# Performance work log

Measured on AMD Instinct MI355X. Metric: run time of the kernel, lower is better.

Reference implementation:

```python
import jax, jax.numpy as jnp
import numpy as np

D_MODEL = 1024
D_HEAD = 64


def setup_inputs() -> dict:
    key = jax.random.key(0)
    k_x, k_q, k_k, k_v, k_o = jax.random.split(key, 5)
    scale = 1.0 / np.sqrt(D_MODEL)
    residual_stream = jax.random.normal(k_x, (4, 2048, D_MODEL), dtype=jnp.float32)
    Q = scale * jax.random.normal(k_q, (D_MODEL, D_HEAD), dtype=jnp.float32)
    K = scale * jax.random.normal(k_k, (D_MODEL, D_HEAD), dtype=jnp.float32)
    V = scale * jax.random.normal(k_v, (D_MODEL, D_HEAD), dtype=jnp.float32)
    O = scale * jax.random.normal(k_o, (D_MODEL, D_HEAD), dtype=jnp.float32)
    return {"residual_stream": residual_stream, "Q": Q, "K": K, "V": V, "O": O}


def reference(residual_stream, Q, K, V, O) -> jnp.ndarray:
    # queries/keys: [B, S, d_head]
    queries = jnp.einsum('bsd,dh->bsh', residual_stream, Q)
    keys = jnp.einsum('bsd,dh->bsh', residual_stream, K)
    # NOTE: original module applies NO 1/sqrt(d_head) scaling.
    pre_attention = jnp.einsum('bqh,bkh->bqk', queries, keys)  # [B, S, S]
    S = pre_attention.shape[-1]
    causal = jnp.tril(jnp.ones((S, S), dtype=bool))
    pre_attention = jnp.where(causal[None], pre_attention, -jnp.inf)
    attention = jax.nn.softmax(pre_attention, axis=-1)
    # x = residual @ V @ O^T : [B, S, d_model]
    x = jnp.einsum('bsd,dh,eh->bse', residual_stream, V, O)
    return jnp.einsum('bqk,bke->bqe', attention, x)
```

## Files before the change

kernel.cpp:

```cpp
#include <hip/hip_runtime.h>
#include <hip/hip_bf16.h>
#include <math.h>

#define BATCH 4
#define SEQ   2048
#define DM    1024
#define DH    64
#define NROWS (BATCH*SEQ)
#define PVSPLIT 8

typedef __hip_bfloat16 bf16;
typedef __attribute__((ext_vector_type(8))) short short8;
typedef __attribute__((ext_vector_type(8))) unsigned short ushortx8;
typedef __attribute__((ext_vector_type(4))) float floatx4;

__device__ __forceinline__ ushort f2bf(float f) {
    union { bf16 h; ushort u; } cv;
    cv.h = __float2bfloat16(f);
    return cv.u;
}
__device__ __forceinline__ float bf2f(ushort u) {
    union { unsigned int i; float f; } v; v.i = ((unsigned int)u) << 16; return v.f;
}

__device__ __forceinline__ void load_lds16(const ushort* g, ushort* l) {
    __builtin_amdgcn_global_load_lds(
        (const __attribute__((address_space(1))) unsigned int*)g,
        (__attribute__((address_space(3))) unsigned int*)l, 16, 0, 0);
}

__global__ __launch_bounds__(256) void wprep_kernel(
    const float* __restrict__ Q, const float* __restrict__ K,
    const float* __restrict__ V, const float* __restrict__ O,
    ushort* __restrict__ WhT, ushort* __restrict__ WlT,
    ushort* __restrict__ Oh, ushort* __restrict__ Ol)
{
    int n = blockIdx.x;
    if (n < 192) {
        const float* W = (n < 64) ? Q : (n < 128) ? K : V;
        int c = n & 63;
        for (int k = threadIdx.x; k < DM; k += 256) {
            float w = W[k * DH + c];
            ushort hi = f2bf(w);
            WhT[n * DM + k] = hi;
            WlT[n * DM + k] = f2bf(w - bf2f(hi));
        }
    } else {
        int e0 = (n - 192) << 4;
        for (int idx = threadIdx.x; idx < 16 * DH; idx += 256) {
            int off = (e0 << 6) + idx;
            float w = O[off];
            ushort hi = f2bf(w);
            Oh[off] = hi;
            Ol[off] = f2bf(w - bf2f(hi));
        }
    }
}

__global__ __launch_bounds__(256) void qkv_part_kernel(
    const float* __restrict__ x, const ushort* __restrict__ WhT,
    const ushort* __restrict__ WlT, float* __restrict__ Cpart)
{
    __shared__ __align__(16) ushort Xs[2][32][34];
    __shared__ __align__(16) ushort Ws[2][192][34];
    int s0 = blockIdx.x * 32;
    int kb = blockIdx.y * 256;
    int t = threadIdx.x;
    int wave = t >> 6, lane = t & 63, m_ = lane & 15, qd = lane >> 4;
    const floatx4 z4 = {0.f, 0.f, 0.f, 0.f};
    floatx4 accq[2] = {z4, z4}, acck[2] = {z4, z4}, accv[2] = {z4, z4};
    int xr = t >> 3, xc = (t & 7) * 4;
    for (int k0 = 0; k0 < 256; k0 += 32) {
        float4 v = *(const float4*)&x[(size_t)(s0 + xr) * DM + kb + k0 + xc];
        ushort h0 = f2bf(v.x), h1 = f2bf(v.y), h2 = f2bf(v.z), h3 = f2bf(v.w);
        *(ushort4*)&Xs[0][xr][xc] = make_ushort4(h0, h1, h2, h3);
        *(ushort4*)&Xs[1][xr][xc] = make_ushort4(
            f2bf(v.x - bf2f(h0)), f2bf(v.y - bf2f(h1)),
            f2bf(v.z - bf2f(h2)), f2bf(v.w - bf2f(h3)));
        #pragma unroll
        for (int j = 0; j < 3; ++j) {
            int idx = t + j * 256, n = idx >> 2, kc = (idx & 3) * 8;
            *(uint4*)&Ws[0][n][kc] = *(const uint4*)&WhT[n * DM + kb + k0 + kc];
            *(uint4*)&Ws[1][n][kc] = *(const uint4*)&WlT[n * DM + kb + k0 + kc];
        }
        __syncthreads();
        short8 ah[2], al[2];
        #pragma unroll
        for (int mi = 0; mi < 2; ++mi) {
            ah[mi] = *(const short8*)&Xs[0][mi * 16 + m_][qd * 8];
            al[mi] = *(const short8*)&Xs[1][mi * 16 + m_][qd * 8];
        }
        int nq = wave * 16 + m_, nk = 64 + wave * 16 + m_, nv = 128 + wave * 16 + m_;
        short8 bqh = *(const short8*)&Ws[0][nq][qd * 8];
        short8 bql = *(const short8*)&Ws[1][nq][qd * 8];
        short8 bkh = *(const short8*)&Ws[0][nk][qd * 8];
        short8 bkl = *(const short8*)&Ws[1][nk][qd * 8];
        short8 bvh = *(const short8*)&Ws[0][nv][qd * 8];
        #pragma unroll
        for (int mi = 0; mi < 2; ++mi) {
            accq[mi] = __builtin_amdgcn_mfma_f32_16x16x32_bf16(ah[mi], bqh, accq[mi], 0, 0, 0);
            accq[mi] = __builtin_amdgcn_mfma_f32_16x16x32_bf16(al[mi], bqh, accq[mi], 0, 0, 0);
            accq[mi] = __builtin_amdgcn_mfma_f32_16x16x32_bf16(ah[mi], bql, accq[mi], 0, 0, 0);
            acck[mi] = __builtin_amdgcn_mfma_f32_16x16x32_bf16(ah[mi], bkh, acck[mi], 0, 0, 0);
            acck[mi] = __builtin_amdgcn_mfma_f32_16x16x32_bf16(al[mi], bkh, acck[mi], 0, 0, 0);
            acck[mi] = __builtin_amdgcn_mfma_f32_16x16x32_bf16(ah[mi], bkl, acck[mi], 0, 0, 0);
            accv[mi] = __builtin_amdgcn_mfma_f32_16x16x32_bf16(ah[mi], bvh, accv[mi], 0, 0, 0);
        }
        __syncthreads();
    }
    float* Cp = Cpart + (size_t)blockIdx.y * (NROWS * 192);
    #pragma unroll
    for (int mi = 0; mi < 2; ++mi) {
        #pragma unroll
        for (int r = 0; r < 4; ++r) {
            int row = s0 + mi * 16 + qd * 4 + r;
            float* base = Cp + (size_t)row * 192;
            base[wave * 16 + m_]       = accq[mi][r];
            base[64 + wave * 16 + m_]  = acck[mi][r];
            base[128 + wave * 16 + m_] = accv[mi][r];
        }
    }
}

__global__ __launch_bounds__(256) void qkv_reduce_kernel(
    const float* __restrict__ Cpart,
    ushort* __restrict__ qh, ushort* __restrict__ ql,
    ushort* __restrict__ kh, ushort* __restrict__ kl, ushort* __restrict__ xvP)
{
    __shared__ ushort xvs[32][72];
    const size_t SL = (size_t)NROWS * 192;
    int row0 = blockIdx.x * 32;
    int t = threadIdx.x;
    #pragma unroll
    for (int i = 0; i < 24; ++i) {
        int e = i * 256 + t;
        int r = e / 192, c = e - r * 192;
        size_t row = row0 + r;
        size_t off = row * 192 + c;
        float s = Cpart[off] + Cpart[SL + off] + Cpart[2 * SL + off] + Cpart[3 * SL + off];
        ushort hi = f2bf(s);
        if (c < 64) {
            qh[row * 64 + c] = hi; ql[row * 64 + c] = f2bf(s - bf2f(hi));
        } else if (c < 128) {
            kh[row * 64 + c - 64] = hi; kl[row * 64 + c - 64] = f2bf(s - bf2f(hi));
        } else {
            xvs[r][c - 128] = hi;
        }
    }
    __syncthreads();
    int h = t & 63, qd = t >> 6;
    ushortx8 v;
    #pragma unroll
    for (int j = 0; j < 8; ++j)
        v[j] = xvs[4 * qd + (j & 3) + ((j >> 2) << 4)][h];
    int b = row0 >> 11, c32 = (row0 & 2047) >> 5;
    *(ushortx8*)&xvP[((((size_t)b << 6) + c32) * 4 + qd) * 512 + h * 8] = v;
}

__global__ __launch_bounds__(512) void attn_part_kernel(
    const ushort* __restrict__ qh, const ushort* __restrict__ ql,
    const ushort* __restrict__ kh, const ushort* __restrict__ kl,
    const ushort* __restrict__ xvP,
    float* __restrict__ Opart, float* __restrict__ lpart)
{
    __shared__ __align__(16) ushort Kbuf[2][8192];
    __shared__ __align__(16) ushort xvbuf[2][4096];
    __shared__ float lred[2][2][16];
    int bid = blockIdx.x;
    int pp = bid & 63, b = (bid >> 6) & 3, s = bid >> 8;
    int srowA = pp << 4, srowB = (127 - pp) << 4;
    int t = threadIdx.x, wave = t >> 6, lane = t & 63, m_ = lane & 15, qd = lane >> 4;
    int nA = (pp >> 2) + 1, nB = ((127 - pp) >> 2) + 1;
    int tile = wave >> 2, h2 = (wave >> 1) & 1, nh = wave & 1;
    int srow = tile ? srowB : srowA;
    int nT = tile ? nB : nA;
    int jB = (nB - s + 3) >> 2;
    const ushort* khb = kh + (((size_t)b << 11)) * 64;
    const ushort* klb = kl + (((size_t)b << 11)) * 64;
    const ushort* xvPb = xvP + ((size_t)b << 17);
    short8 bq[2][2];
    {
        size_t qr = (size_t)((b << 11) + srow + m_) * 64 + qd * 8;
        bq[0][0] = *(const short8*)&qh[qr];
        bq[0][1] = *(const short8*)&qh[qr + 32];
        bq[1][0] = *(const short8*)&ql[qr];
        bq[1][1] = *(const short8*)&ql[qr + 32];
    }
    int drow = lane >> 3;
    int dlc = ((lane & 7) ^ drow) * 8;
    #define AT_STAGE(cc, buf)                                                   \
        { int k0r_ = (cc) << 6;                                                 \
          _Pragma("unroll")                                                     \
          for (int i_ = 0; i_ < 3; ++i_) {                                      \
              int c_ = wave * 3 + i_;                                           \
              if (c_ < 8)                                                       \
                  load_lds16(khb + (size_t)(k0r_ + c_ * 8 + drow) * 64 + dlc,   \
                             &Kbuf[buf][c_ * 512]);                             \
              else if (c_ < 16)                                                 \
                  load_lds16(klb + (size_t)(k0r_ + (c_ - 8) * 8 + drow) * 64 + dlc, \
                             &Kbuf[buf][4096 + (c_ - 8) * 512]);                \
              else                                                              \
                  load_lds16(xvPb + (size_t)(cc) * 4096 + (c_ - 16) * 512 + lane * 8, \
                             &xvbuf[buf][(c_ - 16) * 512]);                     \
          } }
    const floatx4 z4 = {0.f, 0.f, 0.f, 0.f};
    floatx4 accO[2] = {z4, z4};
    float ll = 0.f;
    int qrow = srow + m_;
    AT_STAGE(s, 0)
    for (int j = 0; j < jB; ++j) {
        int c = s + 4 * j;
        __syncthreads();
        if (j + 1 < jB) AT_STAGE(s + 4 * (j + 1), (j + 1) & 1)
        if (c < nT) {
            int bufi = j & 1;
            floatx4 accS[2] = {z4, z4};
            #pragma unroll
            for (int kk = 0; kk < 2; ++kk) {
                #pragma unroll
                for (int tt = 0; tt < 2; ++tt) {
                    int row = (2 * h2 + tt) * 16 + m_;
                    int chunk = ((kk << 2) + qd) ^ (m_ & 7);
                    const ushort* ph = &Kbuf[bufi][row * 64 + chunk * 8];
                    short8 akh = *(const short8*)ph;
                    short8 akl = *(const short8*)(ph + 4096);
                    accS[tt] = __builtin_amdgcn_mfma_f32_16x16x32_bf16(akh, bq[0][kk], accS[tt], 0, 0, 0);
                    accS[tt] = __builtin_amdgcn_mfma_f32_16x16x32_bf16(akl, bq[0][kk], accS[tt], 0, 0, 0);
                    accS[tt] = __builtin_amdgcn_mfma_f32_16x16x32_bf16(akh, bq[1][kk], accS[tt], 0, 0, 0);
                }
            }
            float lsum = 0.f;
            short8 pa;
            #pragma unroll
            for (int tt = 0; tt < 2; ++tt) {
                #pragma unroll
                for (int r = 0; r < 4; ++r) {
                    int kc = c * 64 + (2 * h2 + tt) * 16 + qd * 4 + r;
                    float p = (kc <= qrow) ? __expf(accS[tt][r]) : 0.f;
                    lsum += p;
                    pa[tt * 4 + r] = (short)f2bf(p);
                }
            }
            if (nh == 0) ll += lsum;
            const ushort* Xb = &xvbuf[bufi][(h2 * 4 + qd) * 512];
            #pragma unroll
            for (int i = 0; i < 2; ++i) {
                int h = (nh * 2 + i) * 16 + m_;
                short8 xv = *(const short8*)&Xb[h * 8];
                accO[i] = __builtin_amdgcn_mfma_f32_16x16x32_bf16(pa, xv, accO[i], 0, 0, 0);
            }
        }
    }
    ll += __shfl_xor(ll, 16); ll += __shfl_xor(ll, 32);
    if (qd == 0 && nh == 0) lred[tile][h2][m_] = ll;
    __syncthreads();
    if (t < 32) {
        int tl = t >> 4, q = t & 15;
        int row = (b << 11) + (tl ? srowB : srowA) + q;
        lpart[(size_t)s * NROWS + row] = lred[tl][0][q] + lred[tl][1][q];
    }
    float* OP = Opart + ((size_t)(s * 2 + h2) * NROWS + (b << 11) + srow) * 64;
    #pragma unroll
    for (int i = 0; i < 2; ++i)
        #pragma unroll
        for (int r = 0; r < 4; ++r)
            OP[(qd * 4 + r) * 64 + (nh * 2 + i) * 16 + m_] = accO[i][r];
    #undef AT_STAGE
}

__global__ __launch_bounds__(256) void axv_reduce_kernel(
    const float* __restrict__ AxvPart, const float* __restrict__ lpart,
    ushort* __restrict__ Axvh, ushort* __restrict__ Axvl)
{
    const size_t PSL = (size_t)NROWS * DH;
    int idx = blockIdx.x * 256 + threadIdx.x;
    size_t e = (size_t)idx * 4;
    int r = (int)(e >> 6);
    float4 a = *(const float4*)&AxvPart[e];
    #pragma unroll
    for (int sp = 1; sp < PVSPLIT; ++sp) {
        float4 v = *(const float4*)&AxvPart[sp * PSL + e];
        a.x += v.x; a.y += v.y; a.z += v.z; a.w += v.w;
    }
    float sc = 1.f / (lpart[r] + lpart[NROWS + r]
                    + lpart[2 * NROWS + r] + lpart[3 * NROWS + r]);
    a.x *= sc; a.y *= sc; a.z *= sc; a.w *= sc;
    ushort h0 = f2bf(a.x), h1 = f2bf(a.y), h2 = f2bf(a.z), h3 = f2bf(a.w);
    *(ushort4*)&Axvh[e] = make_ushort4(h0, h1, h2, h3);
    *(ushort4*)&Axvl[e] = make_ushort4(
        f2bf(a.x - bf2f(h0)), f2bf(a.y - bf2f(h1)),
        f2bf(a.z - bf2f(h2)), f2bf(a.w - bf2f(h3)));
}

__global__ __launch_bounds__(256) void out_kernel(
    const ushort* __restrict__ Axvh, const ushort* __restrict__ Axvl,
    const ushort* __restrict__ Oh, const ushort* __restrict__ Ol,
    float* __restrict__ out)
{
    __shared__ __align__(16) ushort As[2][64][72];
    __shared__ __align__(16) ushort Bsh[2][128][72];
    int bid = blockIdx.x;
    int r0 = (bid >> 3) << 6;
    int e0 = (bid & 7) << 7;
    int t = threadIdx.x;
    {
        int tr = t >> 2, tc = (t & 3) << 4;
        const ushort* ah = Axvh + (size_t)(r0 + tr) * DH + tc;
        const ushort* al = Axvl + (size_t)(r0 + tr) * DH + tc;
        *(uint4*)&As[0][tr][tc]     = *(const uint4*)ah;
        *(uint4*)&As[0][tr][tc + 8] = *(const uint4*)(ah + 8);
        *(uint4*)&As[1][tr][tc]     = *(const uint4*)al;
        *(uint4*)&As[1][tr][tc + 8] = *(const uint4*)(al + 8);
    }
    {
        int tr = t >> 1, tc = (t & 1) << 5;
        const ushort* bh = Oh + (size_t)(e0 + tr) * DH + tc;
        const ushort* bl = Ol + (size_t)(e0 + tr) * DH + tc;
        *(uint4*)&Bsh[0][tr][tc]      = *(const uint4*)bh;
        *(uint4*)&Bsh[0][tr][tc + 8]  = *(const uint4*)(bh + 8);
        *(uint4*)&Bsh[0][tr][tc + 16] = *(const uint4*)(bh + 16);
        *(uint4*)&Bsh[0][tr][tc + 24] = *(const uint4*)(bh + 24);
        *(uint4*)&Bsh[1][tr][tc]      = *(const uint4*)bl;
        *(uint4*)&Bsh[1][tr][tc + 8]  = *(const uint4*)(bl + 8);
        *(uint4*)&Bsh[1][tr][tc + 16] = *(const uint4*)(bl + 16);
        *(uint4*)&Bsh[1][tr][tc + 24] = *(const uint4*)(bl + 24);
    }
    __syncthreads();
    int wave = t >> 6, lane = t & 63, m_ = lane & 15, qd = lane >> 4;
    const floatx4 z4 = {0.f, 0.f, 0.f, 0.f};
    floatx4 acc[8] = {z4, z4, z4, z4, z4, z4, z4, z4};
    #pragma unroll
    for (int kk = 0; kk < 2; ++kk) {
        short8 ah = *(const short8*)&As[0][wave * 16 + m_][kk * 32 + qd * 8];
        short8 al = *(const short8*)&As[1][wave * 16 + m_][kk * 32 + qd * 8];
        #pragma unroll
        for (int ni = 0; ni < 8; ++ni) {
            short8 bh = *(const short8*)&Bsh[0][ni * 16 + m_][kk * 32 + qd * 8];
            short8 bl = *(const short8*)&Bsh[1][ni * 16 + m_][kk * 32 + qd * 8];
            acc[ni] = __builtin_amdgcn_mfma_f32_16x16x32_bf16(ah, bh, acc[ni], 0, 0, 0);
            acc[ni] = __builtin_amdgcn_mfma_f32_16x16x32_bf16(al, bh, acc[ni], 0, 0, 0);
            acc[ni] = __builtin_amdgcn_mfma_f32_16x16x32_bf16(ah, bl, acc[ni], 0, 0, 0);
        }
    }
    #pragma unroll
    for (int r = 0; r < 4; ++r) {
        int row = r0 + wave * 16 + qd * 4 + r;
        float* orow = out + (size_t)row * DM + e0;
        #pragma unroll
        for (int ni = 0; ni < 8; ++ni)
            orow[ni * 16 + m_] = acc[ni][r];
    }
}

extern "C" void kernel_launch(void* const* d_in, const int* in_sizes, int n_in,
                              void* d_out, int out_size, void* d_ws, size_t ws_size,
                              hipStream_t stream) {
    const float* x = (const float*)d_in[0];
    const float* Q = (const float*)d_in[1];
    const float* K = (const float*)d_in[2];
    const float* V = (const float*)d_in[3];
    const float* O = (const float*)d_in[4];
    float* out = (float*)d_out;

    char* ws = (char*)d_ws;
    ushort* qh   = (ushort*)(ws);
    ushort* ql   = (ushort*)(ws + (1ull  << 20));
    ushort* kh   = (ushort*)(ws + (2ull  << 20));
    ushort* kl   = (ushort*)(ws + (3ull  << 20));
    ushort* xvP  = (ushort*)(ws + (4ull  << 20));
    ushort* WhT  = (ushort*)(ws + (5ull  << 20));
    ushort* WlT  = (ushort*)(ws + (5ull  << 20) + (512ull << 10));
    float*  lpart = (float*)(ws + (6ull  << 20));
    ushort* Oh   = (ushort*)(ws + (6ull  << 20) + (256ull << 10));
    ushort* Ol   = (ushort*)(ws + (6ull  << 20) + (384ull << 10));
    float*  Opart = (float*)(ws + (7ull << 20));
    float*  Cpart = (float*)(ws + (23ull << 20));
    ushort* Axvh = qh;
    ushort* Axvl = ql;

    wprep_kernel<<<256, 256, 0, stream>>>(Q, K, V, O, WhT, WlT, Oh, Ol);
    qkv_part_kernel<<<dim3(NROWS / 32, 4), 256, 0, stream>>>(x, WhT, WlT, Cpart);
    qkv_reduce_kernel<<<NROWS / 32, 256, 0, stream>>>(Cpart, qh, ql, kh, kl, xvP);
    attn_part_kernel<<<64 * BATCH * 4, 512, 0, stream>>>(qh, ql, kh, kl, xvP, Opart, lpart);
    axv_reduce_kernel<<<NROWS * DH / 4 / 256, 256, 0, stream>>>(Opart, lpart, Axvh, Axvl);
    out_kernel<<<(NROWS / 64) * 8, 256, 0, stream>>>(Axvh, Axvl, Oh, Ol, out);
}
```

Baseline: 160.2 us.

## Fuse QKV split-K reduction and output reduction into their consumer GEMM kernels

```diff
diff --git a/kernel.cpp b/kernel.cpp
--- a/kernel.cpp
+++ b/kernel.cpp
@@ -7,7 +7,6 @@
 #define DM    1024
 #define DH    64
 #define NROWS (BATCH*SEQ)
-#define PVSPLIT 8
 
 typedef __hip_bfloat16 bf16;
 typedef __attribute__((ext_vector_type(8))) short short8;
@@ -57,104 +56,70 @@
     }
 }
 
-__global__ __launch_bounds__(256) void qkv_part_kernel(
+__global__ __launch_bounds__(512) void qkv_fused_kernel(
     const float* __restrict__ x, const ushort* __restrict__ WhT,
-    const ushort* __restrict__ WlT, float* __restrict__ Cpart)
+    const ushort* __restrict__ WlT,
+    ushort* __restrict__ qh, ushort* __restrict__ ql,
+    ushort* __restrict__ kh, ushort* __restrict__ kl, ushort* __restrict__ xvP)
 {
     __shared__ __align__(16) ushort Xs[2][32][34];
     __shared__ __align__(16) ushort Ws[2][192][34];
     int s0 = blockIdx.x * 32;
-    int kb = blockIdx.y * 256;
     int t = threadIdx.x;
     int wave = t >> 6, lane = t & 63, m_ = lane & 15, qd = lane >> 4;
+    int mh = wave >> 2, cg = wave & 3;
     const floatx4 z4 = {0.f, 0.f, 0.f, 0.f};
-    floatx4 accq[2] = {z4, z4}, acck[2] = {z4, z4}, accv[2] = {z4, z4};
-    int xr = t >> 3, xc = (t & 7) * 4;
-    for (int k0 = 0; k0 < 256; k0 += 32) {
-        float4 v = *(const float4*)&x[(size_t)(s0 + xr) * DM + kb + k0 + xc];
-        ushort h0 = f2bf(v.x), h1 = f2bf(v.y), h2 = f2bf(v.z), h3 = f2bf(v.w);
-        *(ushort4*)&Xs[0][xr][xc] = make_ushort4(h0, h1, h2, h3);
-        *(ushort4*)&Xs[1][xr][xc] = make_ushort4(
-            f2bf(v.x - bf2f(h0)), f2bf(v.y - bf2f(h1)),
-            f2bf(v.z - bf2f(h2)), f2bf(v.w - bf2f(h3)));
+    floatx4 accq = z4, acck = z4, accv = z4;
+    int xr = t >> 4, xc = (t & 15) * 2;
+    for (int k0 = 0; k0 < 1024; k0 += 32) {
+        float2 v = *(const float2*)&x[(size_t)(s0 + xr) * DM + k0 + xc];
+        ushort h0 = f2bf(v.x), h1 = f2bf(v.y);
+        *(ushort2*)&Xs[0][xr][xc] = make_ushort2(h0, h1);
+        *(ushort2*)&Xs[1][xr][xc] = make_ushort2(
+            f2bf(v.x - bf2f(h0)), f2bf(v.y - bf2f(h1)));
         #pragma unroll
         for (int j = 0; j < 3; ++j) {
-            int idx = t + j * 256, n = idx >> 2, kc = (idx & 3) * 8;
-            *(uint4*)&Ws[0][n][kc] = *(const uint4*)&WhT[n * DM + kb + k0 + kc];
-            *(uint4*)&Ws[1][n][kc] = *(const uint4*)&WlT[n * DM + kb + k0 + kc];
+            int idx = t + j * 512;
+            int hl = (idx >= 768);
+            int r2 = idx - hl * 768;
+            int n = r2 >> 2, kc = (r2 & 3) * 8;
+            const ushort* src = hl ? WlT : WhT;
+            *(uint4*)&Ws[hl][n][kc] = *(const uint4*)&src[n * DM + k0 + kc];
         }
         __syncthreads();
-        short8 ah[2], al[2];
-        #pragma unroll
-        for (int mi = 0; mi < 2; ++mi) {
-            ah[mi] = *(const short8*)&Xs[0][mi * 16 + m_][qd * 8];
-            al[mi] = *(const short8*)&Xs[1][mi * 16 + m_][qd * 8];
-        }
-        int nq = wave * 16 + m_, nk = 64 + wave * 16 + m_, nv = 128 + wave * 16 + m_;
+        short8 ah = *(const short8*)&Xs[0][mh * 16 + m_][qd * 8];
+        short8 al = *(const short8*)&Xs[1][mh * 16 + m_][qd * 8];
+        int nq = cg * 16 + m_, nk = 64 + cg * 16 + m_, nv = 128 + cg * 16 + m_;
         short8 bqh = *(const short8*)&Ws[0][nq][qd * 8];
         short8 bql = *(const short8*)&Ws[1][nq][qd * 8];
         short8 bkh = *(const short8*)&Ws[0][nk][qd * 8];
         short8 bkl = *(const short8*)&Ws[1][nk][qd * 8];
         short8 bvh = *(const short8*)&Ws[0][nv][qd * 8];
-        #pragma unroll
-        for (int mi = 0; mi < 2; ++mi) {
-            accq[mi] = __builtin_amdgcn_mfma_f32_16x16x32_bf16(ah[mi], bqh, accq[mi], 0, 0, 0);
-            accq[mi] = __builtin_amdgcn_mfma_f32_16x16x32_bf16(al[mi], bqh, accq[mi], 0, 0, 0);
-            accq[mi] = __builtin_amdgcn_mfma_f32_16x16x32_bf16(ah[mi], bql, accq[mi], 0, 0, 0);
-            acck[mi] = __builtin_amdgcn_mfma_f32_16x16x32_bf16(ah[mi], bkh, acck[mi], 0, 0, 0);
-            acck[mi] = __builtin_amdgcn_mfma_f32_16x16x32_bf16(al[mi], bkh, acck[mi], 0, 0, 0);
-            acck[mi] = __builtin_amdgcn_mfma_f32_16x16x32_bf16(ah[mi], bkl, acck[mi], 0, 0, 0);
-            accv[mi] = __builtin_amdgcn_mfma_f32_16x16x32_bf16(ah[mi], bvh, accv[mi], 0, 0, 0);
-        }
+        accq = __builtin_amdgcn_mfma_f32_16x16x32_bf16(ah, bqh, accq, 0, 0, 0);
+        accq = __builtin_amdgcn_mfma_f32_16x16x32_bf16(al, bqh, accq, 0, 0, 0);
+        accq = __builtin_amdgcn_mfma_f32_16x16x32_bf16(ah, bql, accq, 0, 0, 0);
+        acck = __builtin_amdgcn_mfma_f32_16x16x32_bf16(ah, bkh, acck, 0, 0, 0);
+        acck = __builtin_amdgcn_mfma_f32_16x16x32_bf16(al, bkh, acck, 0, 0, 0);
+        acck = __builtin_amdgcn_mfma_f32_16x16x32_bf16(ah, bkl, acck, 0, 0, 0);
+        accv = __builtin_amdgcn_mfma_f32_16x16x32_bf16(ah, bvh, accv, 0, 0, 0);
         __syncthreads();
     }
-    float* Cp = Cpart + (size_t)blockIdx.y * (NROWS * 192);
-    #pragma unroll
-    for (int mi = 0; mi < 2; ++mi) {
-        #pragma unroll
-        for (int r = 0; r < 4; ++r) {
-            int row = s0 + mi * 16 + qd * 4 + r;
-            float* base = Cp + (size_t)row * 192;
-            base[wave * 16 + m_]       = accq[mi][r];
-            base[64 + wave * 16 + m_]  = acck[mi][r];
-            base[128 + wave * 16 + m_] = accv[mi][r];
-        }
-    }
-}
-
-__global__ __launch_bounds__(256) void qkv_reduce_kernel(
-    const float* __restrict__ Cpart,
-    ushort* __restrict__ qh, ushort* __restrict__ ql,
-    ushort* __restrict__ kh, ushort* __restrict__ kl, ushort* __restrict__ xvP)
-{
-    __shared__ ushort xvs[32][72];
-    const size_t SL = (size_t)NROWS * 192;
-    int row0 = blockIdx.x * 32;
-    int t = threadIdx.x;
-    #pragma unroll
-    for (int i = 0; i < 24; ++i) {
-        int e = i * 256 + t;
-        int r = e / 192, c = e - r * 192;
-        size_t row = row0 + r;
-        size_t off = row * 192 + c;
-        float s = Cpart[off] + Cpart[SL + off] + Cpart[2 * SL + off] + Cpart[3 * SL + off];
-        ushort hi = f2bf(s);
-        if (c < 64) {
-            qh[row * 64 + c] = hi; ql[row * 64 + c] = f2bf(s - bf2f(hi));
-        } else if (c < 128) {
-            kh[row * 64 + c - 64] = hi; kl[row * 64 + c - 64] = f2bf(s - bf2f(hi));
-        } else {
-            xvs[r][c - 128] = hi;
-        }
-    }
-    __syncthreads();
-    int h = t & 63, qd = t >> 6;
-    ushortx8 v;
-    #pragma unroll
-    for (int j = 0; j < 8; ++j)
-        v[j] = xvs[4 * qd + (j & 3) + ((j >> 2) << 4)][h];
-    int b = row0 >> 11, c32 = (row0 & 2047) >> 5;
-    *(ushortx8*)&xvP[((((size_t)b << 6) + c32) * 4 + qd) * 512 + h * 8] = v;
+    int col = cg * 16 + m_;
+    #pragma unroll
+    for (int r = 0; r < 4; ++r) {
+        int row = s0 + mh * 16 + qd * 4 + r;
+        ushort hq = f2bf(accq[r]);
+        qh[row * 64 + col] = hq;
+        ql[row * 64 + col] = f2bf(accq[r] - bf2f(hq));
+        ushort hk = f2bf(acck[r]);
+        kh[row * 64 + col] = hk;
+        kl[row * 64 + col] = f2bf(acck[r] - bf2f(hk));
+    }
+    int b = s0 >> 11, c32 = (s0 & 2047) >> 5;
+    ushort4 v4;
+    v4.x = f2bf(accv[0]); v4.y = f2bf(accv[1]);
+    v4.z = f2bf(accv[2]); v4.w = f2bf(accv[3]);
+    *(ushort4*)&xvP[(size_t)(((b * 64 + c32) * 4 + qd) * 512) + col * 8 + mh * 4] = v4;
 }
 
 __global__ __launch_bounds__(512) void attn_part_kernel(
@@ -268,84 +233,65 @@
     #undef AT_STAGE
 }
 
-__global__ __launch_bounds__(256) void axv_reduce_kernel(
-    const float* __restrict__ AxvPart, const float* __restrict__ lpart,
-    ushort* __restrict__ Axvh, ushort* __restrict__ Axvl)
-{
-    const size_t PSL = (size_t)NROWS * DH;
-    int idx = blockIdx.x * 256 + threadIdx.x;
-    size_t e = (size_t)idx * 4;
-    int r = (int)(e >> 6);
-    float4 a = *(const float4*)&AxvPart[e];
-    #pragma unroll
-    for (int sp = 1; sp < PVSPLIT; ++sp) {
-        float4 v = *(const float4*)&AxvPart[sp * PSL + e];
-        a.x += v.x; a.y += v.y; a.z += v.z; a.w += v.w;
-    }
-    float sc = 1.f / (lpart[r] + lpart[NROWS + r]
-                    + lpart[2 * NROWS + r] + lpart[3 * NROWS + r]);
-    a.x *= sc; a.y *= sc; a.z *= sc; a.w *= sc;
-    ushort h0 = f2bf(a.x), h1 = f2bf(a.y), h2 = f2bf(a.z), h3 = f2bf(a.w);
-    *(ushort4*)&Axvh[e] = make_ushort4(h0, h1, h2, h3);
-    *(ushort4*)&Axvl[e] = make_ushort4(
-        f2bf(a.x - bf2f(h0)), f2bf(a.y - bf2f(h1)),
-        f2bf(a.z - bf2f(h2)), f2bf(a.w - bf2f(h3)));
-}
-
-__global__ __launch_bounds__(256) void out_kernel(
-    const ushort* __restrict__ Axvh, const ushort* __restrict__ Axvl,
+__global__ __launch_bounds__(512) void out_fused_kernel(
+    const float* __restrict__ Opart, const float* __restrict__ lpart,
     const ushort* __restrict__ Oh, const ushort* __restrict__ Ol,
     float* __restrict__ out)
 {
-    __shared__ __align__(16) ushort As[2][64][72];
-    __shared__ __align__(16) ushort Bsh[2][128][72];
-    int bid = blockIdx.x;
-    int r0 = (bid >> 3) << 6;
-    int e0 = (bid & 7) << 7;
+    __shared__ float Axv[16][68];
+    __shared__ float lsc[16];
+    int r0 = blockIdx.x * 16;
     int t = threadIdx.x;
+    if (t < 16) {
+        int rg = r0 + t;
+        lsc[t] = 1.f / (lpart[rg] + lpart[NROWS + rg]
+                      + lpart[2 * NROWS + rg] + lpart[3 * NROWS + rg]);
+    }
+    __syncthreads();
     {
-        int tr = t >> 2, tc = (t & 3) << 4;
-        const ushort* ah = Axvh + (size_t)(r0 + tr) * DH + tc;
-        const ushort* al = Axvl + (size_t)(r0 + tr) * DH + tc;
-        *(uint4*)&As[0][tr][tc]     = *(const uint4*)ah;
-        *(uint4*)&As[0][tr][tc + 8] = *(const uint4*)(ah + 8);
-        *(uint4*)&As[1][tr][tc]     = *(const uint4*)al;
-        *(uint4*)&As[1][tr][tc + 8] = *(const uint4*)(al + 8);
-    }
-    {
-        int tr = t >> 1, tc = (t & 1) << 5;
-        const ushort* bh = Oh + (size_t)(e0 + tr) * DH + tc;
-        const ushort* bl = Ol + (size_t)(e0 + tr) * DH + tc;
-        *(uint4*)&Bsh[0][tr][tc]      = *(const uint4*)bh;
-        *(uint4*)&Bsh[0][tr][tc + 8]  = *(const uint4*)(bh + 8);
-        *(uint4*)&Bsh[0][tr][tc + 16] = *(const uint4*)(bh + 16);
-        *(uint4*)&Bsh[0][tr][tc + 24] = *(const uint4*)(bh + 24);
-        *(uint4*)&Bsh[1][tr][tc]      = *(const uint4*)bl;
-        *(uint4*)&Bsh[1][tr][tc + 8]  = *(const uint4*)(bl + 8);
-        *(uint4*)&Bsh[1][tr][tc + 16] = *(const uint4*)(bl + 16);
-        *(uint4*)&Bsh[1][tr][tc + 24] = *(const uint4*)(bl + 24);
+        const size_t PSL = (size_t)NROWS * DH;
+        size_t e = (size_t)r0 * 64 + t * 2;
+        float2 a = *(const float2*)&Opart[e];
+        #pragma unroll
+        for (int sp = 1; sp < 8; ++sp) {
+            float2 w = *(const float2*)&Opart[sp * PSL + e];
+            a.x += w.x; a.y += w.y;
+        }
+        int rr = t >> 5;
+        float sc = lsc[rr];
+        Axv[rr][(t & 31) * 2]     = a.x * sc;
+        Axv[rr][(t & 31) * 2 + 1] = a.y * sc;
     }
     __syncthreads();
     int wave = t >> 6, lane = t & 63, m_ = lane & 15, qd = lane >> 4;
+    int e0w = wave << 7;
+    short8 Ah[2], Al[2];
+    #pragma unroll
+    for (int kk = 0; kk < 2; ++kk)
+        #pragma unroll
+        for (int j = 0; j < 8; ++j) {
+            float vv = Axv[m_][kk * 32 + qd * 8 + j];
+            ushort hv = f2bf(vv);
+            Ah[kk][j] = (short)hv;
+            Al[kk][j] = (short)f2bf(vv - bf2f(hv));
+        }
     const floatx4 z4 = {0.f, 0.f, 0.f, 0.f};
     floatx4 acc[8] = {z4, z4, z4, z4, z4, z4, z4, z4};
     #pragma unroll
-    for (int kk = 0; kk < 2; ++kk) {
-        short8 ah = *(const short8*)&As[0][wave * 16 + m_][kk * 32 + qd * 8];
-        short8 al = *(const short8*)&As[1][wave * 16 + m_][kk * 32 + qd * 8];
-        #pragma unroll
-        for (int ni = 0; ni < 8; ++ni) {
-            short8 bh = *(const short8*)&Bsh[0][ni * 16 + m_][kk * 32 + qd * 8];
-            short8 bl = *(const short8*)&Bsh[1][ni * 16 + m_][kk * 32 + qd * 8];
-            acc[ni] = __builtin_amdgcn_mfma_f32_16x16x32_bf16(ah, bh, acc[ni], 0, 0, 0);
-            acc[ni] = __builtin_amdgcn_mfma_f32_16x16x32_bf16(al, bh, acc[ni], 0, 0, 0);
-            acc[ni] = __builtin_amdgcn_mfma_f32_16x16x32_bf16(ah, bl, acc[ni], 0, 0, 0);
+    for (int ni = 0; ni < 8; ++ni) {
+        #pragma unroll
+        for (int kk = 0; kk < 2; ++kk) {
+            size_t boff = (size_t)(e0w + ni * 16 + m_) * 64 + kk * 32 + qd * 8;
+            short8 bh = *(const short8*)&Oh[boff];
+            short8 bl = *(const short8*)&Ol[boff];
+            acc[ni] = __builtin_amdgcn_mfma_f32_16x16x32_bf16(Ah[kk], bh, acc[ni], 0, 0, 0);
+            acc[ni] = __builtin_amdgcn_mfma_f32_16x16x32_bf16(Al[kk], bh, acc[ni], 0, 0, 0);
+            acc[ni] = __builtin_amdgcn_mfma_f32_16x16x32_bf16(Ah[kk], bl, acc[ni], 0, 0, 0);
         }
     }
     #pragma unroll
     for (int r = 0; r < 4; ++r) {
-        int row = r0 + wave * 16 + qd * 4 + r;
-        float* orow = out + (size_t)row * DM + e0;
+        float* orow = out + (size_t)(r0 + qd * 4 + r) * DM + e0w;
         #pragma unroll
         for (int ni = 0; ni < 8; ++ni)
             orow[ni * 16 + m_] = acc[ni][r];
@@ -374,14 +320,9 @@
     ushort* Oh   = (ushort*)(ws + (6ull  << 20) + (256ull << 10));
     ushort* Ol   = (ushort*)(ws + (6ull  << 20) + (384ull << 10));
     float*  Opart = (float*)(ws + (7ull << 20));
-    float*  Cpart = (float*)(ws + (23ull << 20));
-    ushort* Axvh = qh;
-    ushort* Axvl = ql;
 
     wprep_kernel<<<256, 256, 0, stream>>>(Q, K, V, O, WhT, WlT, Oh, Ol);
-    qkv_part_kernel<<<dim3(NROWS / 32, 4), 256, 0, stream>>>(x, WhT, WlT, Cpart);
-    qkv_reduce_kernel<<<NROWS / 32, 256, 0, stream>>>(Cpart, qh, ql, kh, kl, xvP);
+    qkv_fused_kernel<<<NROWS / 32, 512, 0, stream>>>(x, WhT, WlT, qh, ql, kh, kl, xvP);
     attn_part_kernel<<<64 * BATCH * 4, 512, 0, stream>>>(qh, ql, kh, kl, xvP, Opart, lpart);
-    axv_reduce_kernel<<<NROWS * DH / 4 / 256, 256, 0, stream>>>(Opart, lpart, Axvh, Axvl);
-    out_kernel<<<(NROWS / 64) * 8, 256, 0, stream>>>(Axvh, Axvl, Oh, Ol, out);
-}
+    out_fused_kernel<<<NROWS / 16, 512, 0, stream>>>(Opart, lpart, Oh, Ol, out);
+}
```

Result: slower. 171.8 us (+7.3%).

## Fuse split-PV reduction and bf16 split into output projection kernel

Applied to the files above, without the earlier changes.

```diff
diff --git a/kernel.cpp b/kernel.cpp
--- a/kernel.cpp
+++ b/kernel.cpp
@@ -7,7 +7,6 @@
 #define DM    1024
 #define DH    64
 #define NROWS (BATCH*SEQ)
-#define PVSPLIT 8
 
 typedef __hip_bfloat16 bf16;
 typedef __attribute__((ext_vector_type(8))) short short8;
@@ -268,84 +267,65 @@
     #undef AT_STAGE
 }
 
-__global__ __launch_bounds__(256) void axv_reduce_kernel(
-    const float* __restrict__ AxvPart, const float* __restrict__ lpart,
-    ushort* __restrict__ Axvh, ushort* __restrict__ Axvl)
-{
-    const size_t PSL = (size_t)NROWS * DH;
-    int idx = blockIdx.x * 256 + threadIdx.x;
-    size_t e = (size_t)idx * 4;
-    int r = (int)(e >> 6);
-    float4 a = *(const float4*)&AxvPart[e];
-    #pragma unroll
-    for (int sp = 1; sp < PVSPLIT; ++sp) {
-        float4 v = *(const float4*)&AxvPart[sp * PSL + e];
-        a.x += v.x; a.y += v.y; a.z += v.z; a.w += v.w;
-    }
-    float sc = 1.f / (lpart[r] + lpart[NROWS + r]
-                    + lpart[2 * NROWS + r] + lpart[3 * NROWS + r]);
-    a.x *= sc; a.y *= sc; a.z *= sc; a.w *= sc;
-    ushort h0 = f2bf(a.x), h1 = f2bf(a.y), h2 = f2bf(a.z), h3 = f2bf(a.w);
-    *(ushort4*)&Axvh[e] = make_ushort4(h0, h1, h2, h3);
-    *(ushort4*)&Axvl[e] = make_ushort4(
-        f2bf(a.x - bf2f(h0)), f2bf(a.y - bf2f(h1)),
-        f2bf(a.z - bf2f(h2)), f2bf(a.w - bf2f(h3)));
-}
-
-__global__ __launch_bounds__(256) void out_kernel(
-    const ushort* __restrict__ Axvh, const ushort* __restrict__ Axvl,
+__global__ __launch_bounds__(512) void out_fused_kernel(
+    const float* __restrict__ Opart, const float* __restrict__ lpart,
     const ushort* __restrict__ Oh, const ushort* __restrict__ Ol,
     float* __restrict__ out)
 {
-    __shared__ __align__(16) ushort As[2][64][72];
-    __shared__ __align__(16) ushort Bsh[2][128][72];
-    int bid = blockIdx.x;
-    int r0 = (bid >> 3) << 6;
-    int e0 = (bid & 7) << 7;
+    __shared__ float Axv[16][68];
+    __shared__ float lsc[16];
+    int r0 = blockIdx.x * 16;
     int t = threadIdx.x;
+    if (t < 16) {
+        int rg = r0 + t;
+        lsc[t] = 1.f / (lpart[rg] + lpart[NROWS + rg]
+                      + lpart[2 * NROWS + rg] + lpart[3 * NROWS + rg]);
+    }
+    __syncthreads();
     {
-        int tr = t >> 2, tc = (t & 3) << 4;
-        const ushort* ah = Axvh + (size_t)(r0 + tr) * DH + tc;
-        const ushort* al = Axvl + (size_t)(r0 + tr) * DH + tc;
-        *(uint4*)&As[0][tr][tc]     = *(const uint4*)ah;
-        *(uint4*)&As[0][tr][tc + 8] = *(const uint4*)(ah + 8);
-        *(uint4*)&As[1][tr][tc]     = *(const uint4*)al;
-        *(uint4*)&As[1][tr][tc + 8] = *(const uint4*)(al + 8);
-    }
-    {
-        int tr = t >> 1, tc = (t & 1) << 5;
-        const ushort* bh = Oh + (size_t)(e0 + tr) * DH + tc;
-        const ushort* bl = Ol + (size_t)(e0 + tr) * DH + tc;
-        *(uint4*)&Bsh[0][tr][tc]      = *(const uint4*)bh;
-        *(uint4*)&Bsh[0][tr][tc + 8]  = *(const uint4*)(bh + 8);
-        *(uint4*)&Bsh[0][tr][tc + 16] = *(const uint4*)(bh + 16);
-        *(uint4*)&Bsh[0][tr][tc + 24] = *(const uint4*)(bh + 24);
-        *(uint4*)&Bsh[1][tr][tc]      = *(const uint4*)bl;
-        *(uint4*)&Bsh[1][tr][tc + 8]  = *(const uint4*)(bl + 8);
-        *(uint4*)&Bsh[1][tr][tc + 16] = *(const uint4*)(bl + 16);
-        *(uint4*)&Bsh[1][tr][tc + 24] = *(const uint4*)(bl + 24);
+        const size_t PSL = (size_t)NROWS * DH;
+        size_t e = (size_t)r0 * 64 + t * 2;
+        float2 a = *(const float2*)&Opart[e];
+        #pragma unroll
+        for (int sp = 1; sp < 8; ++sp) {
+            float2 w = *(const float2*)&Opart[sp * PSL + e];
+            a.x += w.x; a.y += w.y;
+        }
+        int rr = t >> 5;
+        float sc = lsc[rr];
+        Axv[rr][(t & 31) * 2]     = a.x * sc;
+        Axv[rr][(t & 31) * 2 + 1] = a.y * sc;
     }
     __syncthreads();
     int wave = t >> 6, lane = t & 63, m_ = lane & 15, qd = lane >> 4;
+    int e0w = wave << 7;
+    short8 Ah[2], Al[2];
+    #pragma unroll
+    for (int kk = 0; kk < 2; ++kk)
+        #pragma unroll
+        for (int j = 0; j < 8; ++j) {
+            float vv = Axv[m_][kk * 32 + qd * 8 + j];
+            ushort hv = f2bf(vv);
+            Ah[kk][j] = (short)hv;
+            Al[kk][j] = (short)f2bf(vv - bf2f(hv));
+        }
     const floatx4 z4 = {0.f, 0.f, 0.f, 0.f};
     floatx4 acc[8] = {z4, z4, z4, z4, z4, z4, z4, z4};
     #pragma unroll
-    for (int kk = 0; kk < 2; ++kk) {
-        short8 ah = *(const short8*)&As[0][wave * 16 + m_][kk * 32 + qd * 8];
-        short8 al = *(const short8*)&As[1][wave * 16 + m_][kk * 32 + qd * 8];
-        #pragma unroll
-        for (int ni = 0; ni < 8; ++ni) {
-            short8 bh = *(const short8*)&Bsh[0][ni * 16 + m_][kk * 32 + qd * 8];
-            short8 bl = *(const short8*)&Bsh[1][ni * 16 + m_][kk * 32 + qd * 8];
-            acc[ni] = __builtin_amdgcn_mfma_f32_16x16x32_bf16(ah, bh, acc[ni], 0, 0, 0);
-            acc[ni] = __builtin_amdgcn_mfma_f32_16x16x32_bf16(al, bh, acc[ni], 0, 0, 0);
-            acc[ni] = __builtin_amdgcn_mfma_f32_16x16x32_bf16(ah, bl, acc[ni], 0, 0, 0);
+    for (int ni = 0; ni < 8; ++ni) {
+        #pragma unroll
+        for (int kk = 0; kk < 2; ++kk) {
+            size_t boff = (size_t)(e0w + ni * 16 + m_) * 64 + kk * 32 + qd * 8;
+            short8 bh = *(const short8*)&Oh[boff];
+            short8 bl = *(const short8*)&Ol[boff];
+            acc[ni] = __builtin_amdgcn_mfma_f32_16x16x32_bf16(Ah[kk], bh, acc[ni], 0, 0, 0);
+            acc[ni] = __builtin_amdgcn_mfma_f32_16x16x32_bf16(Al[kk], bh, acc[ni], 0, 0, 0);
+            acc[ni] = __builtin_amdgcn_mfma_f32_16x16x32_bf16(Ah[kk], bl, acc[ni], 0, 0, 0);
         }
     }
     #pragma unroll
     for (int r = 0; r < 4; ++r) {
-        int row = r0 + wave * 16 + qd * 4 + r;
-        float* orow = out + (size_t)row * DM + e0;
+        float* orow = out + (size_t)(r0 + qd * 4 + r) * DM + e0w;
         #pragma unroll
         for (int ni = 0; ni < 8; ++ni)
             orow[ni * 16 + m_] = acc[ni][r];
@@ -375,13 +355,10 @@
     ushort* Ol   = (ushort*)(ws + (6ull  << 20) + (384ull << 10));
     float*  Opart = (float*)(ws + (7ull << 20));
     float*  Cpart = (float*)(ws + (23ull << 20));
-    ushort* Axvh = qh;
-    ushort* Axvl = ql;
 
     wprep_kernel<<<256, 256, 0, stream>>>(Q, K, V, O, WhT, WlT, Oh, Ol);
     qkv_part_kernel<<<dim3(NROWS / 32, 4), 256, 0, stream>>>(x, WhT, WlT, Cpart);
     qkv_reduce_kernel<<<NROWS / 32, 256, 0, stream>>>(Cpart, qh, ql, kh, kl, xvP);
     attn_part_kernel<<<64 * BATCH * 4, 512, 0, stream>>>(qh, ql, kh, kl, xvP, Opart, lpart);
-    axv_reduce_kernel<<<NROWS * DH / 4 / 256, 256, 0, stream>>>(Opart, lpart, Axvh, Axvl);
-    out_kernel<<<(NROWS / 64) * 8, 256, 0, stream>>>(Axvh, Axvl, Oh, Ol, out);
-}
+    out_fused_kernel<<<NROWS / 16, 512, 0, stream>>>(Opart, lpart, Oh, Ol, out);
+}
```

Measured after the change: 169.7 us. 5.9% more time.
